# Kernel tuning notes

Measured on AMD Instinct MI355X. Metric: run time of the kernel, lower is better.

The kernel has to match this reference:

```python
import jax, jax.numpy as jnp
import numpy as np

P, B, N, M, D_LAT = 4, 32, 2048, 512, 128
BETA = 1e-3
BIG = 1e9  # sentinel for masked-out pairwise distances


def quat_to_rotmat(q):
    # q: (..., 4) quaternion (w, x, y, z), normalized then converted
    q = q / jnp.linalg.norm(q, axis=-1, keepdims=True)
    w, x, y, z = q[..., 0], q[..., 1], q[..., 2], q[..., 3]
    R = jnp.stack([
        1 - 2 * (y * y + z * z), 2 * (x * y - w * z), 2 * (x * z + w * y),
        2 * (x * y + w * z), 1 - 2 * (x * x + z * z), 2 * (y * z - w * x),
        2 * (x * z - w * y), 2 * (y * z + w * x), 1 - 2 * (x * x + y * y),
    ], axis=-1)
    return R.reshape(q.shape[:-1] + (3, 3))


def setup_inputs() -> dict:
    key = jax.random.key(0)
    ks = jax.random.split(key, 8)
    return {
        'ipt': jax.random.normal(ks[0], (B, N, 3), jnp.float32),
        'opt': jax.random.normal(ks[1], (P, B, M, 3), jnp.float32),
        'trans': jax.random.normal(ks[2], (P, B, 3), jnp.float32),
        'rots': jax.random.normal(ks[3], (P, B, 4), jnp.float32),
        'probs': jax.random.uniform(ks[4], (P, B, 1), jnp.float32),
        'idx': jax.random.randint(ks[5], (B, N), 0, P),
        'mu': jax.random.normal(ks[6], (B, D_LAT), jnp.float32),
        'logvar': jax.random.normal(ks[7], (B, D_LAT), jnp.float32),
    }


def _parts_distance(ipt, opt, trans, rots, probs, idx):
    # Masked, fully-batched equivalent of the original python double loop:
    # index_select by (idx==i) + _remove_zero_rows are expressed as boolean
    # masks; empty part/sample combinations are excluded via `valid`.
    chamfer_d = 0.0
    coverage = 0.0
    quality = 0.0
    num = 0.0
    nonzero_x = jnp.any(ipt != 0, axis=-1)  # (B, N)
    for i in range(P):  # fixed small part count, structurally distinct slices
        y = opt[i]                                   # (B, M, 3)
        mask_y = jnp.any(y != 0, axis=-1)            # (B, M) _remove_zero_rows
        mx = (idx == i) & nonzero_x                  # (B, N) part selection
        # transform_to_primitives_centric_system: x_local = R (x - t)
        R = quat_to_rotmat(rots[i])                  # (B, 3, 3)
        x = jnp.einsum('bij,bnj->bni', R, ipt - trans[i][:, None, :])
        # pairwise squared distances, (B, N, M)
        D = jnp.sum((x[:, :, None, :] - y[:, None, :, :]) ** 2, axis=-1)
        nx = jnp.sum(mx, axis=-1)                    # (B,)
        ny = jnp.sum(mask_y, axis=-1)                # (B,)
        # quality: mean over valid x of min distance to valid y
        qual = jnp.sum(jnp.where(mx, jnp.min(jnp.where(mask_y[:, None, :], D, BIG), axis=-1), 0.0), axis=-1) / jnp.maximum(nx, 1)
        # coverage: mean over valid y of min distance to valid x
        cov = jnp.sum(jnp.where(mask_y, jnp.min(jnp.where(mx[:, :, None], D, BIG), axis=-2), 0.0), axis=-1) / jnp.maximum(ny, 1)
        cd = qual + cov                              # symmetric chamfer
        valid = (nx > 0) & (ny > 0)                  # x.size(0)!=0 and y.size(0)!=0
        w = jnp.where(valid, probs[i][:, 0], 0.0)    # prob-weighted sum over batch
        n = jnp.sum(valid).astype(jnp.float32)
        has = (n > 0).astype(jnp.float32)
        inv_n = has / jnp.maximum(n, 1.0)
        chamfer_d = chamfer_d + jnp.sum(w * cd) * inv_n
        coverage = coverage + jnp.sum(w * cov) * inv_n
        quality = quality + jnp.sum(w * qual) * inv_n
        num = num + has
    inv_num = 1.0 / jnp.maximum(num, 1.0)
    return chamfer_d * inv_num, coverage * inv_num, quality * inv_num


def KL(mu, logvar):
    # standard VAE KL: sum over latent, mean over batch
    return -0.5 * jnp.sum(1.0 + logvar - mu ** 2 - jnp.exp(logvar)) / mu.shape[0]


def reference(ipt, opt, trans, rots, probs, idx, mu, logvar):
    cds, covs, quals = _parts_distance(ipt, opt, trans, rots, probs, idx)
    kld = KL(mu, logvar)
    return (cds + BETA * kld, cds, covs, quals, kld)
```

## Files before the change

### kernel.cpp

```cpp
#include <hip/hip_runtime.h>
#include <math.h>

#define PP 4
#define BB 32
#define PB (PP * BB)
#define NN 2048
#define MM 512
#define DLAT 128
#define BETA_C 1e-3f
#define BIGV 1e9f
#define SENT 1e8f
#define THREADS 512
#define NWAVE 8
#define QCHUNKS 4
#define CCHUNKS 4
#define QCH (NN / QCHUNKS)
#define CCH (MM / CCHUNKS)
#define XMAX (NN + 32)

__device__ float g_ws[16 * PB];

__device__ __forceinline__ int wave_compact_slot(bool sel, int* s_cnt, int lane) {
    unsigned long long bal = __ballot(sel);
    int lofs = __popcll(bal & ((1ull << lane) - 1ull));
    int base = 0;
    if (lane == 0 && bal) base = atomicAdd(s_cnt, __popcll(bal));
    base = __shfl(base, 0);
    return base + lofs;
}

__global__ __launch_bounds__(THREADS, 8) void parts_kernel(
    const float* __restrict__ ipt,
    const float* __restrict__ opt,
    const float* __restrict__ trans,
    const float* __restrict__ rots,
    const int*   __restrict__ idx)
{
    const int b = blockIdx.x;
    const int i = blockIdx.y;
    const int z = blockIdx.z;
    const int tid = threadIdx.x;
    const int lane = tid & 63;
    const int w = tid >> 6;

    __shared__ float Rm[12];
    __shared__ int s_nx, s_ny;
    __shared__ __align__(16) float syx[MM], syy[MM], syz[MM];
    __shared__ __align__(16) float sxx[XMAX], sxy[XMAX], sxz[XMAX];
    __shared__ float pmin[NWAVE][128];
    __shared__ float red[NWAVE];

    if (tid == 0) {
        s_nx = 0;
        s_ny = 0;
        const float* q = rots + (i * BB + b) * 4;
        float qw = q[0], qx = q[1], qy = q[2], qz = q[3];
        float inv = 1.0f / sqrtf(qw * qw + qx * qx + qy * qy + qz * qz);
        qw *= inv; qx *= inv; qy *= inv; qz *= inv;
        Rm[0] = 1.0f - 2.0f * (qy * qy + qz * qz);
        Rm[1] = 2.0f * (qx * qy - qw * qz);
        Rm[2] = 2.0f * (qx * qz + qw * qy);
        Rm[3] = 2.0f * (qx * qy + qw * qz);
        Rm[4] = 1.0f - 2.0f * (qx * qx + qz * qz);
        Rm[5] = 2.0f * (qy * qz - qw * qx);
        Rm[6] = 2.0f * (qx * qz - qw * qy);
        Rm[7] = 2.0f * (qy * qz + qw * qx);
        Rm[8] = 1.0f - 2.0f * (qx * qx + qy * qy);
        const float* t = trans + (i * BB + b) * 3;
        Rm[9] = t[0]; Rm[10] = t[1]; Rm[11] = t[2];
    }
    __syncthreads();

    const float R0 = Rm[0], R1 = Rm[1], R2 = Rm[2];
    const float R3 = Rm[3], R4 = Rm[4], R5 = Rm[5];
    const float R6 = Rm[6], R7 = Rm[7], R8 = Rm[8];
    const float t0 = Rm[9], t1 = Rm[10], t2 = Rm[11];
    const size_t optbase = ((size_t)i * BB + b) * MM;
    const int pb = i * BB + b;

    float sum = 0.0f;

    if (z < QCHUNKS) {
        for (int m = tid; m < MM; m += THREADS) {
            const float* y = opt + (optbase + m) * 3;
            float yx = y[0], yy = y[1], yz = y[2];
            bool v = (yx != 0.0f) | (yy != 0.0f) | (yz != 0.0f);
            if (!v) { yx = SENT; yy = SENT; yz = SENT; }
            syx[m] = yx; syy[m] = yy; syz[m] = yz;
        }
        const int n0 = z * QCH;
        for (int n = n0 + tid; n < n0 + QCH; n += THREADS) {
            const float* p = ipt + ((size_t)b * NN + n) * 3;
            float px = p[0], py = p[1], pz = p[2];
            bool nz = (px != 0.0f) | (py != 0.0f) | (pz != 0.0f);
            bool sel = nz && (idx[b * NN + n] == i);
            int pos = wave_compact_slot(sel, &s_nx, lane);
            if (sel) {
                px -= t0; py -= t1; pz -= t2;
                sxx[pos] = R0 * px + R1 * py + R2 * pz;
                sxy[pos] = R3 * px + R4 * py + R5 * pz;
                sxz[pos] = R6 * px + R7 * py + R8 * pz;
            }
        }
        __syncthreads();
        const int nxc = s_nx;
        const int y0 = w * (MM / NWAVE);

        for (int base = 0; base < nxc; base += 128) {
            float px[2], py[2], pz[2], mn[2];
#pragma unroll
            for (int s = 0; s < 2; ++s) {
                int k = base + s * 64 + lane;
                bool a = (k < nxc);
                px[s] = a ? sxx[k] : SENT;
                py[s] = a ? sxy[k] : SENT;
                pz[s] = a ? sxz[k] : SENT;
                mn[s] = BIGV;
            }
            for (int j = 0; j < MM / NWAVE; j += 4) {
                float4 yx = *reinterpret_cast<const float4*>(syx + y0 + j);
                float4 yy = *reinterpret_cast<const float4*>(syy + y0 + j);
                float4 yz = *reinterpret_cast<const float4*>(syz + y0 + j);
#pragma unroll
                for (int s = 0; s < 2; ++s) {
                    float dx0 = px[s] - yx.x, dy0 = py[s] - yy.x, dz0 = pz[s] - yz.x;
                    float dx1 = px[s] - yx.y, dy1 = py[s] - yy.y, dz1 = pz[s] - yz.y;
                    float dx2 = px[s] - yx.z, dy2 = py[s] - yy.z, dz2 = pz[s] - yz.z;
                    float dx3 = px[s] - yx.w, dy3 = py[s] - yy.w, dz3 = pz[s] - yz.w;
                    float d0 = dx0 * dx0 + dy0 * dy0 + dz0 * dz0;
                    float d1 = dx1 * dx1 + dy1 * dy1 + dz1 * dz1;
                    float d2 = dx2 * dx2 + dy2 * dy2 + dz2 * dz2;
                    float d3 = dx3 * dx3 + dy3 * dy3 + dz3 * dz3;
                    mn[s] = fminf(mn[s], fminf(fminf(d0, d1), fminf(d2, d3)));
                }
            }
#pragma unroll
            for (int s = 0; s < 2; ++s) pmin[w][s * 64 + lane] = mn[s];
            __syncthreads();
            if (tid < 128 && base + tid < nxc) {
                float m = pmin[0][tid];
#pragma unroll
                for (int ww = 1; ww < NWAVE; ++ww) m = fminf(m, pmin[ww][tid]);
                sum += m;
            }
            __syncthreads();
        }

        for (int off = 32; off > 0; off >>= 1) sum += __shfl_down(sum, off);
        if (lane == 0) red[w] = sum;
        __syncthreads();
        if (tid == 0) {
            float tot = 0.0f;
            for (int ww = 0; ww < NWAVE; ++ww) tot += red[ww];
            g_ws[(0 + z) * PB + pb] = tot;
            g_ws[(8 + z) * PB + pb] = (float)s_nx;
        }
    } else {
        const int c = z - QCHUNKS;
        if (tid < CCH) {
            const float* y = opt + (optbase + c * CCH + tid) * 3;
            float yx = y[0], yy = y[1], yz = y[2];
            bool v = (yx != 0.0f) | (yy != 0.0f) | (yz != 0.0f);
            if (!v) { yx = SENT; yy = SENT; yz = SENT; }
            syx[tid] = yx; syy[tid] = yy; syz[tid] = yz;
            unsigned long long bal = __ballot(v);
            if (lane == 0) atomicAdd(&s_ny, __popcll(bal));
        }
        for (int n = tid; n < NN; n += THREADS) {
            const float* p = ipt + ((size_t)b * NN + n) * 3;
            float px = p[0], py = p[1], pz = p[2];
            bool nz = (px != 0.0f) | (py != 0.0f) | (pz != 0.0f);
            bool sel = nz && (idx[b * NN + n] == i);
            int pos = wave_compact_slot(sel, &s_nx, lane);
            if (sel) {
                px -= t0; py -= t1; pz -= t2;
                sxx[pos] = R0 * px + R1 * py + R2 * pz;
                sxy[pos] = R3 * px + R4 * py + R5 * pz;
                sxz[pos] = R6 * px + R7 * py + R8 * pz;
            }
        }
        __syncthreads();
        const int nx = s_nx;
        const int ny = s_ny;
        const int nx32 = (nx + 31) & ~31;
        if (tid < nx32 - nx) {
            sxx[nx + tid] = SENT; sxy[nx + tid] = SENT; sxz[nx + tid] = SENT;
        }
        __syncthreads();

        float qx[2], qy[2], qz[2], mn[2];
#pragma unroll
        for (int s = 0; s < 2; ++s) {
            int j = s * 64 + lane;
            qx[s] = syx[j]; qy[s] = syy[j]; qz[s] = syz[j];
            mn[s] = BIGV;
        }
        const int q = nx32 / NWAVE;
        const int x0 = w * q;
        for (int k = 0; k < q; k += 4) {
            float4 xx = *reinterpret_cast<const float4*>(sxx + x0 + k);
            float4 xy = *reinterpret_cast<const float4*>(sxy + x0 + k);
            float4 xz = *reinterpret_cast<const float4*>(sxz + x0 + k);
#pragma unroll
            for (int s = 0; s < 2; ++s) {
                float dx0 = qx[s] - xx.x, dy0 = qy[s] - xy.x, dz0 = qz[s] - xz.x;
                float dx1 = qx[s] - xx.y, dy1 = qy[s] - xy.y, dz1 = qz[s] - xz.y;
                float dx2 = qx[s] - xx.z, dy2 = qy[s] - xy.z, dz2 = qz[s] - xz.z;
                float dx3 = qx[s] - xx.w, dy3 = qy[s] - xy.w, dz3 = qz[s] - xz.w;
                float d0 = dx0 * dx0 + dy0 * dy0 + dz0 * dz0;
                float d1 = dx1 * dx1 + dy1 * dy1 + dz1 * dz1;
                float d2 = dx2 * dx2 + dy2 * dy2 + dz2 * dz2;
                float d3 = dx3 * dx3 + dy3 * dy3 + dz3 * dz3;
                mn[s] = fminf(mn[s], fminf(fminf(d0, d1), fminf(d2, d3)));
            }
        }
#pragma unroll
        for (int s = 0; s < 2; ++s) pmin[w][s * 64 + lane] = mn[s];
        __syncthreads();
        if (tid < CCH && syx[tid] != SENT) {
            float m = pmin[0][tid];
#pragma unroll
            for (int ww = 1; ww < NWAVE; ++ww) m = fminf(m, pmin[ww][tid]);
            sum += m;
        }
        __syncthreads();

        for (int off = 32; off > 0; off >>= 1) sum += __shfl_down(sum, off);
        if (lane == 0) red[w] = sum;
        __syncthreads();
        if (tid == 0) {
            float tot = 0.0f;
            for (int ww = 0; ww < NWAVE; ++ww) tot += red[ww];
            g_ws[(4 + c) * PB + pb] = tot;
            g_ws[(12 + c) * PB + pb] = (float)ny;
        }
    }
}

__global__ __launch_bounds__(256) void finalize_kernel(
    const float* __restrict__ probs,
    const float* __restrict__ mu,
    const float* __restrict__ logvar,
    float* __restrict__ out)
{
    const int tid = threadIdx.x;
    __shared__ float red[4];
    __shared__ float s_wq[PB], s_wc[PB], s_val[PB];

    const float4* mu4 = reinterpret_cast<const float4*>(mu);
    const float4* lv4 = reinterpret_cast<const float4*>(logvar);
    float kls = 0.0f;
    for (int t = tid; t < BB * DLAT / 4; t += 256) {
        float4 m4 = mu4[t], l4 = lv4[t];
        kls += (1.0f + l4.x - m4.x * m4.x - expf(l4.x))
             + (1.0f + l4.y - m4.y * m4.y - expf(l4.y))
             + (1.0f + l4.z - m4.z * m4.z - expf(l4.z))
             + (1.0f + l4.w - m4.w * m4.w - expf(l4.w));
    }
    for (int off = 32; off > 0; off >>= 1) kls += __shfl_down(kls, off);
    if ((tid & 63) == 0) red[tid >> 6] = kls;

    if (tid < PB) {
        float qs  = g_ws[0 * PB + tid] + g_ws[1 * PB + tid] + g_ws[2 * PB + tid] + g_ws[3 * PB + tid];
        float cs  = g_ws[4 * PB + tid] + g_ws[5 * PB + tid] + g_ws[6 * PB + tid] + g_ws[7 * PB + tid];
        float nxf = g_ws[8 * PB + tid] + g_ws[9 * PB + tid] + g_ws[10 * PB + tid] + g_ws[11 * PB + tid];
        float nyf = g_ws[12 * PB + tid] + g_ws[13 * PB + tid] + g_ws[14 * PB + tid] + g_ws[15 * PB + tid];
        bool valid = (nxf > 0.0f) && (nyf > 0.0f);
        float wgt = valid ? probs[tid] : 0.0f;
        s_wq[tid] = wgt * (qs / fmaxf(nxf, 1.0f));
        s_wc[tid] = wgt * (cs / fmaxf(nyf, 1.0f));
        s_val[tid] = valid ? 1.0f : 0.0f;
    }
    __syncthreads();

    if (tid == 0) {
        float kld = -0.5f * (red[0] + red[1] + red[2] + red[3]) / (float)BB;
        float ch = 0.0f, cov = 0.0f, qu = 0.0f, num = 0.0f;
        for (int ii = 0; ii < PP; ++ii) {
            float sq = 0.0f, sc = 0.0f, n = 0.0f;
            for (int bb = 0; bb < BB; ++bb) {
                sq += s_wq[ii * BB + bb];
                sc += s_wc[ii * BB + bb];
                n += s_val[ii * BB + bb];
            }
            float has = (n > 0.0f) ? 1.0f : 0.0f;
            float invn = has / fmaxf(n, 1.0f);
            qu += sq * invn;
            cov += sc * invn;
            ch += (sq + sc) * invn;
            num += has;
        }
        float invnum = 1.0f / fmaxf(num, 1.0f);
        float cds = ch * invnum;
        out[0] = cds + BETA_C * kld;
        out[1] = cds;
        out[2] = cov * invnum;
        out[3] = qu * invnum;
        out[4] = kld;
    }
}

extern "C" void kernel_launch(void* const* d_in, const int* in_sizes, int n_in,
                              void* d_out, int out_size, void* d_ws, size_t ws_size,
                              hipStream_t stream) {
    const float* ipt    = (const float*)d_in[0];
    const float* opt    = (const float*)d_in[1];
    const float* trans  = (const float*)d_in[2];
    const float* rots   = (const float*)d_in[3];
    const float* probs  = (const float*)d_in[4];
    const int*   idx    = (const int*)d_in[5];
    const float* mu     = (const float*)d_in[6];
    const float* logvar = (const float*)d_in[7];
    float* out = (float*)d_out;
    (void)d_ws; (void)ws_size; (void)in_sizes; (void)n_in; (void)out_size;

    dim3 grid(BB, PP, QCHUNKS + CCHUNKS);
    parts_kernel<<<grid, THREADS, 0, stream>>>(ipt, opt, trans, rots, idx);
    finalize_kernel<<<1, 256, 0, stream>>>(probs, mu, logvar, out);
}
```

Baseline: 91.78 us.

## Compute both chamfer directions from one distance pass with column-min reduction

```diff
diff --git a/kernel.cpp b/kernel.cpp
--- a/kernel.cpp
+++ b/kernel.cpp
@@ -12,13 +12,16 @@
 #define SENT 1e8f
 #define THREADS 512
 #define NWAVE 8
-#define QCHUNKS 4
-#define CCHUNKS 4
-#define QCH (NN / QCHUNKS)
-#define CCH (MM / CCHUNKS)
-#define XMAX (NN + 32)
-
-__device__ float g_ws[16 * PB];
+#define XCHUNKS 4
+#define QCH (NN / XCHUNKS)
+#define XMAX (QCH + 32)
+
+#define GW_QUAL(z, pb)   ((z) * PB + (pb))
+#define GW_NX(z, pb)     (512 + (z) * PB + (pb))
+#define GW_COV(pb)       (1024 + (pb))
+#define GW_NY(pb)        (1152 + (pb))
+#define GW_COL(z, pb, j) (2048 + (((z) * PB + (pb)) * 512) + (j))
+__device__ float g_ws[2048 + 4 * PB * 512];
 
 __device__ __forceinline__ int wave_compact_slot(bool sel, int* s_cnt, int lane) {
     unsigned long long bal = __ballot(sel);
@@ -44,15 +47,15 @@
     const int w = tid >> 6;
 
     __shared__ float Rm[12];
-    __shared__ int s_nx, s_ny;
+    __shared__ int s_nx;
     __shared__ __align__(16) float syx[MM], syy[MM], syz[MM];
     __shared__ __align__(16) float sxx[XMAX], sxy[XMAX], sxz[XMAX];
     __shared__ float pmin[NWAVE][128];
+    __shared__ float colw[NWAVE][64];
     __shared__ float red[NWAVE];
 
     if (tid == 0) {
         s_nx = 0;
-        s_ny = 0;
         const float* q = rots + (i * BB + b) * 4;
         float qw = q[0], qx = q[1], qy = q[2], qz = q[3];
         float inv = 1.0f / sqrtf(qw * qw + qx * qx + qy * qy + qz * qz);
@@ -69,6 +72,7 @@
         const float* t = trans + (i * BB + b) * 3;
         Rm[9] = t[0]; Rm[10] = t[1]; Rm[11] = t[2];
     }
+    colw[w][lane] = BIGV;
     __syncthreads();
 
     const float R0 = Rm[0], R1 = Rm[1], R2 = Rm[2];
@@ -78,162 +82,130 @@
     const size_t optbase = ((size_t)i * BB + b) * MM;
     const int pb = i * BB + b;
 
+    {
+        const float* y = opt + (optbase + tid) * 3;
+        float yx = y[0], yy = y[1], yz = y[2];
+        bool v = (yx != 0.0f) | (yy != 0.0f) | (yz != 0.0f);
+        if (!v) { yx = SENT; yy = SENT; yz = SENT; }
+        syx[tid] = yx; syy[tid] = yy; syz[tid] = yz;
+    }
+    {
+        const int n = z * QCH + tid;
+        const float* p = ipt + ((size_t)b * NN + n) * 3;
+        float px = p[0], py = p[1], pz = p[2];
+        bool nz = (px != 0.0f) | (py != 0.0f) | (pz != 0.0f);
+        bool sel = nz && (idx[b * NN + n] == i);
+        int pos = wave_compact_slot(sel, &s_nx, lane);
+        if (sel) {
+            px -= t0; py -= t1; pz -= t2;
+            sxx[pos] = R0 * px + R1 * py + R2 * pz;
+            sxy[pos] = R3 * px + R4 * py + R5 * pz;
+            sxz[pos] = R6 * px + R7 * py + R8 * pz;
+        }
+    }
+    __syncthreads();
+    const int nxc = s_nx;
+    const int y0 = w * 64;
+
     float sum = 0.0f;
-
-    if (z < QCHUNKS) {
-        for (int m = tid; m < MM; m += THREADS) {
-            const float* y = opt + (optbase + m) * 3;
-            float yx = y[0], yy = y[1], yz = y[2];
-            bool v = (yx != 0.0f) | (yy != 0.0f) | (yz != 0.0f);
-            if (!v) { yx = SENT; yy = SENT; yz = SENT; }
-            syx[m] = yx; syy[m] = yy; syz[m] = yz;
-        }
-        const int n0 = z * QCH;
-        for (int n = n0 + tid; n < n0 + QCH; n += THREADS) {
-            const float* p = ipt + ((size_t)b * NN + n) * 3;
-            float px = p[0], py = p[1], pz = p[2];
-            bool nz = (px != 0.0f) | (py != 0.0f) | (pz != 0.0f);
-            bool sel = nz && (idx[b * NN + n] == i);
-            int pos = wave_compact_slot(sel, &s_nx, lane);
-            if (sel) {
-                px -= t0; py -= t1; pz -= t2;
-                sxx[pos] = R0 * px + R1 * py + R2 * pz;
-                sxy[pos] = R3 * px + R4 * py + R5 * pz;
-                sxz[pos] = R6 * px + R7 * py + R8 * pz;
-            }
-        }
-        __syncthreads();
-        const int nxc = s_nx;
-        const int y0 = w * (MM / NWAVE);
-
-        for (int base = 0; base < nxc; base += 128) {
-            float px[2], py[2], pz[2], mn[2];
+    for (int base = 0; base < nxc; base += 128) {
+        float px[2], py[2], pz[2], mn[2];
+#pragma unroll
+        for (int s = 0; s < 2; ++s) {
+            int k = base + s * 64 + lane;
+            bool a = (k < nxc);
+            px[s] = a ? sxx[k] : SENT;
+            py[s] = a ? sxy[k] : SENT;
+            pz[s] = a ? sxz[k] : SENT;
+            mn[s] = BIGV;
+        }
+        for (int it = 0; it < 16; ++it) {
+            const int j = it * 4;
+            float4 yx = *reinterpret_cast<const float4*>(syx + y0 + j);
+            float4 yy = *reinterpret_cast<const float4*>(syy + y0 + j);
+            float4 yz = *reinterpret_cast<const float4*>(syz + y0 + j);
+            float c0 = BIGV, c1 = BIGV, c2 = BIGV, c3 = BIGV;
 #pragma unroll
             for (int s = 0; s < 2; ++s) {
-                int k = base + s * 64 + lane;
-                bool a = (k < nxc);
-                px[s] = a ? sxx[k] : SENT;
-                py[s] = a ? sxy[k] : SENT;
-                pz[s] = a ? sxz[k] : SENT;
-                mn[s] = BIGV;
-            }
-            for (int j = 0; j < MM / NWAVE; j += 4) {
-                float4 yx = *reinterpret_cast<const float4*>(syx + y0 + j);
-                float4 yy = *reinterpret_cast<const float4*>(syy + y0 + j);
-                float4 yz = *reinterpret_cast<const float4*>(syz + y0 + j);
-#pragma unroll
-                for (int s = 0; s < 2; ++s) {
-                    float dx0 = px[s] - yx.x, dy0 = py[s] - yy.x, dz0 = pz[s] - yz.x;
-                    float dx1 = px[s] - yx.y, dy1 = py[s] - yy.y, dz1 = pz[s] - yz.y;
-                    float dx2 = px[s] - yx.z, dy2 = py[s] - yy.z, dz2 = pz[s] - yz.z;
-                    float dx3 = px[s] - yx.w, dy3 = py[s] - yy.w, dz3 = pz[s] - yz.w;
-                    float d0 = dx0 * dx0 + dy0 * dy0 + dz0 * dz0;
-                    float d1 = dx1 * dx1 + dy1 * dy1 + dz1 * dz1;
-                    float d2 = dx2 * dx2 + dy2 * dy2 + dz2 * dz2;
-                    float d3 = dx3 * dx3 + dy3 * dy3 + dz3 * dz3;
-                    mn[s] = fminf(mn[s], fminf(fminf(d0, d1), fminf(d2, d3)));
-                }
-            }
-#pragma unroll
-            for (int s = 0; s < 2; ++s) pmin[w][s * 64 + lane] = mn[s];
-            __syncthreads();
-            if (tid < 128 && base + tid < nxc) {
-                float m = pmin[0][tid];
-#pragma unroll
-                for (int ww = 1; ww < NWAVE; ++ww) m = fminf(m, pmin[ww][tid]);
-                sum += m;
-            }
-            __syncthreads();
-        }
-
-        for (int off = 32; off > 0; off >>= 1) sum += __shfl_down(sum, off);
-        if (lane == 0) red[w] = sum;
-        __syncthreads();
-        if (tid == 0) {
-            float tot = 0.0f;
-            for (int ww = 0; ww < NWAVE; ++ww) tot += red[ww];
-            g_ws[(0 + z) * PB + pb] = tot;
-            g_ws[(8 + z) * PB + pb] = (float)s_nx;
-        }
-    } else {
-        const int c = z - QCHUNKS;
-        if (tid < CCH) {
-            const float* y = opt + (optbase + c * CCH + tid) * 3;
-            float yx = y[0], yy = y[1], yz = y[2];
-            bool v = (yx != 0.0f) | (yy != 0.0f) | (yz != 0.0f);
-            if (!v) { yx = SENT; yy = SENT; yz = SENT; }
-            syx[tid] = yx; syy[tid] = yy; syz[tid] = yz;
-            unsigned long long bal = __ballot(v);
-            if (lane == 0) atomicAdd(&s_ny, __popcll(bal));
-        }
-        for (int n = tid; n < NN; n += THREADS) {
-            const float* p = ipt + ((size_t)b * NN + n) * 3;
-            float px = p[0], py = p[1], pz = p[2];
-            bool nz = (px != 0.0f) | (py != 0.0f) | (pz != 0.0f);
-            bool sel = nz && (idx[b * NN + n] == i);
-            int pos = wave_compact_slot(sel, &s_nx, lane);
-            if (sel) {
-                px -= t0; py -= t1; pz -= t2;
-                sxx[pos] = R0 * px + R1 * py + R2 * pz;
-                sxy[pos] = R3 * px + R4 * py + R5 * pz;
-                sxz[pos] = R6 * px + R7 * py + R8 * pz;
-            }
-        }
-        __syncthreads();
-        const int nx = s_nx;
-        const int ny = s_ny;
-        const int nx32 = (nx + 31) & ~31;
-        if (tid < nx32 - nx) {
-            sxx[nx + tid] = SENT; sxy[nx + tid] = SENT; sxz[nx + tid] = SENT;
-        }
-        __syncthreads();
-
-        float qx[2], qy[2], qz[2], mn[2];
-#pragma unroll
-        for (int s = 0; s < 2; ++s) {
-            int j = s * 64 + lane;
-            qx[s] = syx[j]; qy[s] = syy[j]; qz[s] = syz[j];
-            mn[s] = BIGV;
-        }
-        const int q = nx32 / NWAVE;
-        const int x0 = w * q;
-        for (int k = 0; k < q; k += 4) {
-            float4 xx = *reinterpret_cast<const float4*>(sxx + x0 + k);
-            float4 xy = *reinterpret_cast<const float4*>(sxy + x0 + k);
-            float4 xz = *reinterpret_cast<const float4*>(sxz + x0 + k);
-#pragma unroll
-            for (int s = 0; s < 2; ++s) {
-                float dx0 = qx[s] - xx.x, dy0 = qy[s] - xy.x, dz0 = qz[s] - xz.x;
-                float dx1 = qx[s] - xx.y, dy1 = qy[s] - xy.y, dz1 = qz[s] - xz.y;
-                float dx2 = qx[s] - xx.z, dy2 = qy[s] - xy.z, dz2 = qz[s] - xz.z;
-                float dx3 = qx[s] - xx.w, dy3 = qy[s] - xy.w, dz3 = qz[s] - xz.w;
+                float dx0 = px[s] - yx.x, dy0 = py[s] - yy.x, dz0 = pz[s] - yz.x;
+                float dx1 = px[s] - yx.y, dy1 = py[s] - yy.y, dz1 = pz[s] - yz.y;
+                float dx2 = px[s] - yx.z, dy2 = py[s] - yy.z, dz2 = pz[s] - yz.z;
+                float dx3 = px[s] - yx.w, dy3 = py[s] - yy.w, dz3 = pz[s] - yz.w;
                 float d0 = dx0 * dx0 + dy0 * dy0 + dz0 * dz0;
                 float d1 = dx1 * dx1 + dy1 * dy1 + dz1 * dz1;
                 float d2 = dx2 * dx2 + dy2 * dy2 + dz2 * dz2;
                 float d3 = dx3 * dx3 + dy3 * dy3 + dz3 * dz3;
                 mn[s] = fminf(mn[s], fminf(fminf(d0, d1), fminf(d2, d3)));
+                c0 = fminf(c0, d0); c1 = fminf(c1, d1);
+                c2 = fminf(c2, d2); c3 = fminf(c3, d3);
+            }
+#pragma unroll
+            for (int m = 1; m < 64; m <<= 1) {
+                c0 = fminf(c0, __shfl_xor(c0, m));
+                c1 = fminf(c1, __shfl_xor(c1, m));
+                c2 = fminf(c2, __shfl_xor(c2, m));
+                c3 = fminf(c3, __shfl_xor(c3, m));
+            }
+            if ((lane >> 2) == it) {
+                int r = lane & 3;
+                float v = (r == 0) ? c0 : (r == 1) ? c1 : (r == 2) ? c2 : c3;
+                colw[w][lane] = fminf(colw[w][lane], v);
             }
         }
 #pragma unroll
         for (int s = 0; s < 2; ++s) pmin[w][s * 64 + lane] = mn[s];
         __syncthreads();
-        if (tid < CCH && syx[tid] != SENT) {
+        if (tid < 128 && base + tid < nxc) {
             float m = pmin[0][tid];
 #pragma unroll
             for (int ww = 1; ww < NWAVE; ++ww) m = fminf(m, pmin[ww][tid]);
             sum += m;
         }
         __syncthreads();
-
-        for (int off = 32; off > 0; off >>= 1) sum += __shfl_down(sum, off);
-        if (lane == 0) red[w] = sum;
-        __syncthreads();
-        if (tid == 0) {
-            float tot = 0.0f;
-            for (int ww = 0; ww < NWAVE; ++ww) tot += red[ww];
-            g_ws[(4 + c) * PB + pb] = tot;
-            g_ws[(12 + c) * PB + pb] = (float)ny;
-        }
+    }
+
+    g_ws[GW_COL(z, pb, y0 + lane)] = colw[w][lane];
+
+    for (int off = 32; off > 0; off >>= 1) sum += __shfl_down(sum, off);
+    if (lane == 0) red[w] = sum;
+    __syncthreads();
+    if (tid == 0) {
+        float tot = 0.0f;
+        for (int ww = 0; ww < NWAVE; ++ww) tot += red[ww];
+        g_ws[GW_QUAL(z, pb)] = tot;
+        g_ws[GW_NX(z, pb)] = (float)nxc;
+    }
+}
+
+__global__ __launch_bounds__(256) void colsum_kernel(
+    const float* __restrict__ opt)
+{
+    const int pb = blockIdx.x;
+    const int tid = threadIdx.x;
+    __shared__ float red[4];
+    __shared__ int redc[4];
+
+    const size_t optbase = (size_t)pb * MM;
+    float sum = 0.0f;
+    int cnt = 0;
+#pragma unroll
+    for (int s = 0; s < 2; ++s) {
+        int j = s * 256 + tid;
+        const float* y = opt + (optbase + j) * 3;
+        bool v = (y[0] != 0.0f) | (y[1] != 0.0f) | (y[2] != 0.0f);
+        float m = fminf(fminf(g_ws[GW_COL(0, pb, j)], g_ws[GW_COL(1, pb, j)]),
+                        fminf(g_ws[GW_COL(2, pb, j)], g_ws[GW_COL(3, pb, j)]));
+        if (v) { sum += m; cnt++; }
+    }
+    for (int off = 32; off > 0; off >>= 1) {
+        sum += __shfl_down(sum, off);
+        cnt += __shfl_down(cnt, off);
+    }
+    if ((tid & 63) == 0) { red[tid >> 6] = sum; redc[tid >> 6] = cnt; }
+    __syncthreads();
+    if (tid == 0) {
+        g_ws[GW_COV(pb)] = red[0] + red[1] + red[2] + red[3];
+        g_ws[GW_NY(pb)] = (float)(redc[0] + redc[1] + redc[2] + redc[3]);
     }
 }
 
@@ -261,10 +233,12 @@
     if ((tid & 63) == 0) red[tid >> 6] = kls;
 
     if (tid < PB) {
-        float qs  = g_ws[0 * PB + tid] + g_ws[1 * PB + tid] + g_ws[2 * PB + tid] + g_ws[3 * PB + tid];
-        float cs  = g_ws[4 * PB + tid] + g_ws[5 * PB + tid] + g_ws[6 * PB + tid] + g_ws[7 * PB + tid];
-        float nxf = g_ws[8 * PB + tid] + g_ws[9 * PB + tid] + g_ws[10 * PB + tid] + g_ws[11 * PB + tid];
-        float nyf = g_ws[12 * PB + tid] + g_ws[13 * PB + tid] + g_ws[14 * PB + tid] + g_ws[15 * PB + tid];
+        float qs  = g_ws[GW_QUAL(0, tid)] + g_ws[GW_QUAL(1, tid)]
+                  + g_ws[GW_QUAL(2, tid)] + g_ws[GW_QUAL(3, tid)];
+        float nxf = g_ws[GW_NX(0, tid)] + g_ws[GW_NX(1, tid)]
+                  + g_ws[GW_NX(2, tid)] + g_ws[GW_NX(3, tid)];
+        float cs  = g_ws[GW_COV(tid)];
+        float nyf = g_ws[GW_NY(tid)];
         bool valid = (nxf > 0.0f) && (nyf > 0.0f);
         float wgt = valid ? probs[tid] : 0.0f;
         s_wq[tid] = wgt * (qs / fmaxf(nxf, 1.0f));
@@ -314,7 +288,8 @@
     float* out = (float*)d_out;
     (void)d_ws; (void)ws_size; (void)in_sizes; (void)n_in; (void)out_size;
 
-    dim3 grid(BB, PP, QCHUNKS + CCHUNKS);
+    dim3 grid(BB, PP, XCHUNKS);
     parts_kernel<<<grid, THREADS, 0, stream>>>(ipt, opt, trans, rots, idx);
+    colsum_kernel<<<PB, 256, 0, stream>>>(opt);
     finalize_kernel<<<1, 256, 0, stream>>>(probs, mu, logvar, out);
 }
```

New measurement: 117.9 us. 1.29x slower.
